# Kernel tuning notes

Hardware: AMD Instinct MI355X
Metric: run time of the kernel (lower is better)

The kernel has to match this reference:

```python
import jax, jax.numpy as jnp
import numpy as np
import math

D_MODEL = 1024
HEADS = 16
D_K = D_MODEL // HEADS
B, S = 4, 2048


def setup_inputs() -> dict:
    key = jax.random.key(0)
    ks = jax.random.split(key, 7)
    scale = 1.0 / math.sqrt(D_MODEL)
    inp = {
        "q": jax.random.normal(ks[0], (B, S, D_MODEL), dtype=jnp.float32),
        "k": jax.random.normal(ks[1], (B, S, D_MODEL), dtype=jnp.float32),
        "v": jax.random.normal(ks[2], (B, S, D_MODEL), dtype=jnp.float32),
        # Linear(d_model, d_model, bias=False) weights, stored [out, in] torch-style
        "W_q": jax.random.normal(ks[3], (D_MODEL, D_MODEL), dtype=jnp.float32) * scale,
        "W_k": jax.random.normal(ks[4], (D_MODEL, D_MODEL), dtype=jnp.float32) * scale,
        "W_v": jax.random.normal(ks[5], (D_MODEL, D_MODEL), dtype=jnp.float32) * scale,
        "W_o": jax.random.normal(ks[6], (D_MODEL, D_MODEL), dtype=jnp.float32) * scale,
    }
    return inp


def reference(q, k, v, W_q, W_k, W_v, W_o):
    # projections (torch Linear: x @ W.T)
    query = jnp.einsum("bsd,ed->bse", q, W_q)
    key_ = jnp.einsum("bsd,ed->bse", k, W_k)
    value = jnp.einsum("bsd,ed->bse", v, W_v)
    # split heads -> [B, H, S, d_k]
    def split(x):
        return x.reshape(B, S, HEADS, D_K).transpose(0, 2, 1, 3)
    Q, K, V = split(query), split(key_), split(value)
    # scaled dot-product attention, full [B,H,S,S] scores (naive, faithful)
    scores = jnp.einsum("bhqd,bhkd->bhqk", Q, K) / math.sqrt(D_K)
    attn = jax.nn.softmax(scores, axis=-1)
    x = jnp.einsum("bhqk,bhkd->bhqd", attn, V)
    x = x.transpose(0, 2, 1, 3).reshape(B, S, D_MODEL)
    return jnp.einsum("bsd,ed->bse", x, W_o)
```

## Files before the change

kernel.cpp:

```cpp
#include <hip/hip_runtime.h>
#include <stdint.h>

#define NHEAD 16
#define DKH 64
#define BBATCH 4
#define SEQ 2048
#define MROWS (BBATCH*SEQ)
#define DMODEL 1024

typedef __attribute__((ext_vector_type(8))) __bf16 bf16x8;
typedef __attribute__((ext_vector_type(4))) float f32x4;

__device__ __forceinline__ unsigned short f2bf(float x) {
  unsigned int u = __float_as_uint(x);
  u += 0x7FFFu + ((u >> 16) & 1u);
  return (unsigned short)(u >> 16);
}
__device__ __forceinline__ unsigned int pkbf(float a, float b) {
  return __builtin_amdgcn_perm(__float_as_uint(b) + 0x8000u,
                               __float_as_uint(a) + 0x8000u, 0x07060302u);
}
__device__ __forceinline__ unsigned int pkbf_t(float a, float b) {
  return __builtin_amdgcn_perm(__float_as_uint(b), __float_as_uint(a), 0x07060302u);
}
__device__ __forceinline__ void gl_lds16(const void* g, void* l) {
  __builtin_amdgcn_global_load_lds(
      (const __attribute__((address_space(1))) unsigned int*)g,
      (__attribute__((address_space(3))) unsigned int*)l, 16, 0, 0);
}
__device__ __forceinline__ f32x4 mfma16(bf16x8 a, bf16x8 b, f32x4 c) {
  return __builtin_amdgcn_mfma_f32_16x16x32_bf16(a, b, c, 0, 0, 0);
}

__global__ __launch_bounds__(256) void cvt_all(
    const float* __restrict__ s0, const float* __restrict__ s1,
    const float* __restrict__ s2, const float* __restrict__ s3,
    const float* __restrict__ s4, const float* __restrict__ s5,
    const float* __restrict__ s6,
    unsigned short* __restrict__ d0, unsigned short* __restrict__ d1,
    unsigned short* __restrict__ d2, unsigned short* __restrict__ d3,
    unsigned short* __restrict__ d4, unsigned short* __restrict__ d5,
    unsigned short* __restrict__ d6) {
  const int NB = 2097152;
  const int NW = 262144;
  int i = blockIdx.x * 256 + threadIdx.x;
  const float* src; unsigned short* dst; int off;
  if      (i < NB)          { src = s0; dst = d0; off = i; }
  else if (i < 2*NB)        { src = s1; dst = d1; off = i - NB; }
  else if (i < 3*NB)        { src = s2; dst = d2; off = i - 2*NB; }
  else if (i < 3*NB + NW)   { src = s3; dst = d3; off = i - 3*NB; }
  else if (i < 3*NB + 2*NW) { src = s4; dst = d4; off = i - 3*NB - NW; }
  else if (i < 3*NB + 3*NW) { src = s5; dst = d5; off = i - 3*NB - 2*NW; }
  else                      { src = s6; dst = d6; off = i - 3*NB - 3*NW; }
  float4 x = ((const float4*)src)[off];
  uint2 o; o.x = pkbf(x.x, x.y); o.y = pkbf(x.z, x.w);
  ((uint2*)dst)[off] = o;
}

__global__ __launch_bounds__(256, 2) void proj_gemm(
    const unsigned short* __restrict__ A0, const unsigned short* __restrict__ A1,
    const unsigned short* __restrict__ A2,
    const unsigned short* __restrict__ B0, const unsigned short* __restrict__ B1,
    const unsigned short* __restrict__ B2,
    unsigned short* __restrict__ O0, unsigned short* __restrict__ O1,
    unsigned short* __restrict__ O2) {
  __shared__ __align__(16) unsigned short smem[2][16384];
  const int z = blockIdx.z;
  const unsigned short* Ah = (z == 0) ? A0 : ((z == 1) ? A1 : A2);
  const unsigned short* Bh = (z == 0) ? B0 : ((z == 1) ? B1 : B2);
  unsigned short* outp = (z == 0) ? O0 : ((z == 1) ? O1 : O2);
  const int t = threadIdx.x;
  const int bm = blockIdx.x, bn = blockIdx.y;
  const int lane = t & 63, lm = lane & 15, quad = lane >> 4;
  const int w = t >> 6, wr = w >> 1, wc = w & 1;

  f32x4 acc[4][4];
#pragma unroll
  for (int i = 0; i < 4; ++i)
#pragma unroll
    for (int j = 0; j < 4; ++j) acc[i][j] = (f32x4){0.f, 0.f, 0.f, 0.f};

  auto stage = [&](int kk, int b) {
#pragma unroll
    for (int jj = 0; jj < 4; ++jj) {
      int cid = jj * 256 + t;
      int r = cid >> 3, c = cid & 7;
      int gcol = kk * 64 + ((c ^ (r & 7)) * 8);
      gl_lds16(Ah + (bm * 128 + r) * 1024 + gcol, &smem[b][cid * 8]);
      gl_lds16(Bh + (bn * 128 + r) * 1024 + gcol, &smem[b][8192 + cid * 8]);
    }
  };

  stage(0, 0);
  __syncthreads();

  for (int kk = 0; kk < 16; ++kk) {
    const int cur = kk & 1;
    if (kk < 15) stage(kk + 1, cur ^ 1);
    const unsigned short* sA = &smem[cur][0];
    const unsigned short* sB = &smem[cur][8192];
#pragma unroll
    for (int kc = 0; kc < 2; ++kc) {
      bf16x8 af[4], bf[4];
#pragma unroll
      for (int i = 0; i < 4; ++i) {
        int m = wr * 64 + i * 16 + lm;
        int nn = wc * 64 + i * 16 + lm;
        int slot = ((kc * 4 + quad) ^ (lm & 7)) * 8;
        af[i] = *(const bf16x8*)(sA + m * 64 + slot);
        bf[i] = *(const bf16x8*)(sB + nn * 64 + slot);
      }
#pragma unroll
      for (int i = 0; i < 4; ++i)
#pragma unroll
        for (int j = 0; j < 4; ++j) acc[i][j] = mfma16(af[i], bf[j], acc[i][j]);
    }
    __syncthreads();
  }

  if (z < 2) {
    float scale = (z == 0) ? 0.125f * 1.44269504f : 1.0f;
#pragma unroll
    for (int i = 0; i < 4; ++i)
#pragma unroll
      for (int j = 0; j < 4; ++j)
#pragma unroll
        for (int r = 0; r < 4; ++r) {
          int m = bm * 128 + wr * 64 + i * 16 + quad * 4 + r;
          int nn = bn * 128 + wc * 64 + j * 16 + lm;
          int b = m >> 11, s = m & 2047, h = nn >> 6, d = nn & 63;
          outp[((b * 16 + h) * 2048 + s) * 64 + d] = f2bf(acc[i][j][r] * scale);
        }
  } else {
    unsigned short* scr = &smem[0][0];
#pragma unroll
    for (int i = 0; i < 4; ++i)
#pragma unroll
      for (int j = 0; j < 4; ++j)
#pragma unroll
        for (int r = 0; r < 4; ++r) {
          int ml = wr * 64 + i * 16 + quad * 4 + r;
          int nl = wc * 64 + j * 16 + lm;
          scr[nl * 128 + (((ml >> 3) ^ (nl & 15)) << 3) + (ml & 7)] =
              f2bf(acc[i][j][r]);
        }
    __syncthreads();
    int nl = t >> 1, half = t & 1;
    int e = bn * 128 + nl, h = e >> 6, d = e & 63;
    int mg = bm * 128;
    int b = mg >> 11, s0 = mg & 2047;
    uint4* dstp = (uint4*)(outp + ((b * 16 + h) * 64 + d) * 2048 + s0);
#pragma unroll
    for (int u = 0; u < 8; ++u) {
      int c = half * 8 + u;
      int slot = c ^ (nl & 15);
      dstp[c] = *(const uint4*)(scr + nl * 128 + slot * 8);
    }
  }
}

__global__ __launch_bounds__(256, 4) void flash_attn(
    const unsigned short* __restrict__ Qw, const unsigned short* __restrict__ Kw,
    const unsigned short* __restrict__ Vt, unsigned short* __restrict__ Xw) {
  __shared__ __align__(16) unsigned short sK[2][64 * 64];
  __shared__ __align__(16) unsigned short sV[2][64 * 64];
  const int t = threadIdx.x;
  const int bh = (blockIdx.x << 3) | blockIdx.z;
  const int qt = blockIdx.y;
  const int lane = t & 63, lm = lane & 15, quad = lane >> 4;
  const int w = t >> 6;

  const unsigned short* gq = Qw + (long)bh * SEQ * 64 + (long)qt * 128 * 64;
  const unsigned short* gk = Kw + (long)bh * SEQ * 64;
  const unsigned short* gv = Vt + (long)bh * 64 * SEQ;

  bf16x8 qf[2][2];
#pragma unroll
  for (int i = 0; i < 2; ++i)
#pragma unroll
    for (int kc = 0; kc < 2; ++kc)
      qf[i][kc] = *(const bf16x8*)(gq + (w * 32 + i * 16 + lm) * 64 + kc * 32 + quad * 8);

  f32x4 o[2][4];
  f32x4 lacc[2];
#pragma unroll
  for (int i = 0; i < 2; ++i) {
    lacc[i] = (f32x4){0.f, 0.f, 0.f, 0.f};
#pragma unroll
    for (int nv = 0; nv < 4; ++nv) o[i][nv] = (f32x4){0.f, 0.f, 0.f, 0.f};
  }

  auto stage = [&](int kt, int b) {
#pragma unroll
    for (int is = 0; is < 2; ++is) {
      int cid = is * 256 + t;
      int rk = cid >> 3, ck = cid & 7;
      int srk = (rk & 3) | ((rk & 8) >> 1);
      gl_lds16(gk + kt * 64 * 64 + rk * 64 + ((ck ^ srk) * 8), &sK[b][cid * 8]);
      int rv = cid >> 3, cv = cid & 7;
      gl_lds16(gv + kt * 64 + rv * SEQ + ((cv ^ (rv & 7)) * 8), &sV[b][cid * 8]);
    }
  };

  uint4 ou; ou.x = ou.y = ou.z = ou.w = 0x3F803F80u;
  const bf16x8 ones = __builtin_bit_cast(bf16x8, ou);

  stage(0, 0);
  __syncthreads();

  for (int kt = 0; kt < 32; ++kt) {
    const int cur = kt & 1;
    if (kt < 31) stage(kt + 1, cur ^ 1);
    const unsigned short* sk = &sK[cur][0];
    const unsigned short* sv = &sV[cur][0];
#pragma unroll
    for (int p = 0; p < 2; ++p) {
      bf16x8 kf[2][2];
#pragma unroll
      for (int tt = 0; tt < 2; ++tt) {
        int g = p * 32 + 8 * (lm >> 2) + (lm & 3) + 4 * tt;
        int sg = (g & 3) | ((g & 8) >> 1);
        kf[tt][0] = *(const bf16x8*)(sk + g * 64 + ((quad ^ sg) * 8));
        kf[tt][1] = *(const bf16x8*)(sk + g * 64 + (((4 + quad) ^ sg) * 8));
      }
      bf16x8 pfrag[2];
#pragma unroll
      for (int i = 0; i < 2; ++i) {
        f32x4 s0 = (f32x4){0.f, 0.f, 0.f, 0.f};
        f32x4 s1 = (f32x4){0.f, 0.f, 0.f, 0.f};
        __builtin_amdgcn_s_setprio(1);
        s0 = mfma16(kf[0][0], qf[i][0], s0);
        s0 = mfma16(kf[0][1], qf[i][1], s0);
        s1 = mfma16(kf[1][0], qf[i][0], s1);
        s1 = mfma16(kf[1][1], qf[i][1], s1);
        __builtin_amdgcn_s_setprio(0);
        float p0[4], p1[4];
#pragma unroll
        for (int r = 0; r < 4; ++r) {
          p0[r] = __builtin_amdgcn_exp2f(s0[r]);
          p1[r] = __builtin_amdgcn_exp2f(s1[r]);
        }
        uint4 pw;
        pw.x = pkbf_t(p0[0], p0[1]); pw.y = pkbf_t(p0[2], p0[3]);
        pw.z = pkbf_t(p1[0], p1[1]); pw.w = pkbf_t(p1[2], p1[3]);
        pfrag[i] = __builtin_bit_cast(bf16x8, pw);
      }
      __builtin_amdgcn_s_setprio(1);
#pragma unroll
      for (int i = 0; i < 2; ++i) lacc[i] = mfma16(pfrag[i], ones, lacc[i]);
#pragma unroll
      for (int nv = 0; nv < 4; ++nv) {
        bf16x8 vb = *(const bf16x8*)(sv + (nv * 16 + lm) * 64 + (((p * 4 + quad) ^ (lm & 7)) * 8));
#pragma unroll
        for (int i = 0; i < 2; ++i) o[i][nv] = mfma16(pfrag[i], vb, o[i][nv]);
      }
      __builtin_amdgcn_s_setprio(0);
    }
    __syncthreads();
  }

  int b = bh >> 4, h = bh & 15;
#pragma unroll
  for (int i = 0; i < 2; ++i) {
    float inv[4];
#pragma unroll
    for (int r = 0; r < 4; ++r) inv[r] = __builtin_amdgcn_rcpf(lacc[i][r]);
#pragma unroll
    for (int nv = 0; nv < 4; ++nv)
#pragma unroll
      for (int r = 0; r < 4; ++r) {
        int q = qt * 128 + w * 32 + i * 16 + quad * 4 + r;
        int d = nv * 16 + lm;
        Xw[((long)(b * 2048 + q) * 16 + h) * 64 + d] = f2bf(o[i][nv][r] * inv[r]);
      }
  }
}

__global__ __launch_bounds__(256, 2) void out_gemm(
    const unsigned short* __restrict__ A, const unsigned short* __restrict__ Bw,
    float* __restrict__ C) {
  __shared__ __align__(16) unsigned short smem[2][16384];
  const int t = threadIdx.x;
  const int bm = blockIdx.x, bn = blockIdx.y;
  const int lane = t & 63, lm = lane & 15, quad = lane >> 4;
  const int w = t >> 6, wr = w >> 1, wc = w & 1;

  f32x4 acc[4][4];
#pragma unroll
  for (int i = 0; i < 4; ++i)
#pragma unroll
    for (int j = 0; j < 4; ++j) acc[i][j] = (f32x4){0.f, 0.f, 0.f, 0.f};

  auto stage = [&](int kk, int b) {
#pragma unroll
    for (int jj = 0; jj < 4; ++jj) {
      int cid = jj * 256 + t;
      int r = cid >> 3, c = cid & 7;
      int gcol = kk * 64 + ((c ^ (r & 7)) * 8);
      gl_lds16(A + (bm * 128 + r) * 1024 + gcol, &smem[b][cid * 8]);
      gl_lds16(Bw + (bn * 128 + r) * 1024 + gcol, &smem[b][8192 + cid * 8]);
    }
  };

  stage(0, 0);
  __syncthreads();

  for (int kk = 0; kk < 16; ++kk) {
    const int cur = kk & 1;
    if (kk < 15) stage(kk + 1, cur ^ 1);
    const unsigned short* sA = &smem[cur][0];
    const unsigned short* sB = &smem[cur][8192];
#pragma unroll
    for (int kc = 0; kc < 2; ++kc) {
      bf16x8 af[4], bf[4];
#pragma unroll
      for (int i = 0; i < 4; ++i) {
        int m = wr * 64 + i * 16 + lm;
        int nn = wc * 64 + i * 16 + lm;
        int slot = ((kc * 4 + quad) ^ (lm & 7)) * 8;
        af[i] = *(const bf16x8*)(sA + m * 64 + slot);
        bf[i] = *(const bf16x8*)(sB + nn * 64 + slot);
      }
#pragma unroll
      for (int i = 0; i < 4; ++i)
#pragma unroll
        for (int j = 0; j < 4; ++j) acc[i][j] = mfma16(af[i], bf[j], acc[i][j]);
    }
    __syncthreads();
  }
#pragma unroll
  for (int i = 0; i < 4; ++i)
#pragma unroll
    for (int j = 0; j < 4; ++j)
#pragma unroll
      for (int r = 0; r < 4; ++r) {
        int m = bm * 128 + wr * 64 + i * 16 + quad * 4 + r;
        int nn = bn * 128 + wc * 64 + j * 16 + lm;
        C[m * 1024 + nn] = acc[i][j][r];
      }
}

extern "C" void kernel_launch(void* const* d_in, const int* in_sizes, int n_in,
                              void* d_out, int out_size, void* d_ws, size_t ws_size,
                              hipStream_t stream) {
  const float* q  = (const float*)d_in[0];
  const float* k  = (const float*)d_in[1];
  const float* v  = (const float*)d_in[2];
  const float* Wq = (const float*)d_in[3];
  const float* Wk = (const float*)d_in[4];
  const float* Wv = (const float*)d_in[5];
  const float* Wo = (const float*)d_in[6];

  char* ws = (char*)d_ws;
  const size_t MK = (size_t)MROWS * DMODEL;
  const size_t KK = (size_t)DMODEL * DMODEL;
  size_t off = 0;
  auto nxt = [&](size_t elems) { unsigned short* p = (unsigned short*)(ws + off); off += elems * 2; return p; };
  unsigned short* q_b  = nxt(MK);
  unsigned short* k_b  = nxt(MK);
  unsigned short* v_b  = nxt(MK);
  unsigned short* Wq_b = nxt(KK);
  unsigned short* Wk_b = nxt(KK);
  unsigned short* Wv_b = nxt(KK);
  unsigned short* Wo_b = nxt(KK);
  unsigned short* Qw = nxt(MK);
  unsigned short* Kw = nxt(MK);
  unsigned short* Vt = nxt(MK);
  unsigned short* Xw = nxt(MK);
  (void)ws_size; (void)in_sizes; (void)n_in; (void)out_size;

  cvt_all<<<28672, 256, 0, stream>>>(q, k, v, Wq, Wk, Wv, Wo,
                                     q_b, k_b, v_b, Wq_b, Wk_b, Wv_b, Wo_b);
  proj_gemm<<<dim3(64, 8, 3), 256, 0, stream>>>(q_b, k_b, v_b,
                                                Wq_b, Wk_b, Wv_b,
                                                Qw, Kw, Vt);
  flash_attn<<<dim3(8, 16, 8), 256, 0, stream>>>(Qw, Kw, Vt, Xw);
  out_gemm<<<dim3(64, 8), 256, 0, stream>>>(Xw, Wo_b, (float*)d_out);
}
```

Baseline: 303.0 us.

## Fuse fp32-to-bf16 activation conversion into projection GEMM A-tile staging

```diff
diff --git a/kernel.cpp b/kernel.cpp
--- a/kernel.cpp
+++ b/kernel.cpp
@@ -32,41 +32,33 @@
   return __builtin_amdgcn_mfma_f32_16x16x32_bf16(a, b, c, 0, 0, 0);
 }
 
-__global__ __launch_bounds__(256) void cvt_all(
-    const float* __restrict__ s0, const float* __restrict__ s1,
-    const float* __restrict__ s2, const float* __restrict__ s3,
-    const float* __restrict__ s4, const float* __restrict__ s5,
-    const float* __restrict__ s6,
-    unsigned short* __restrict__ d0, unsigned short* __restrict__ d1,
-    unsigned short* __restrict__ d2, unsigned short* __restrict__ d3,
-    unsigned short* __restrict__ d4, unsigned short* __restrict__ d5,
-    unsigned short* __restrict__ d6) {
-  const int NB = 2097152;
+__global__ __launch_bounds__(256) void cvt_w(
+    const float* __restrict__ s3, const float* __restrict__ s4,
+    const float* __restrict__ s5, const float* __restrict__ s6,
+    unsigned short* __restrict__ d3, unsigned short* __restrict__ d4,
+    unsigned short* __restrict__ d5, unsigned short* __restrict__ d6) {
   const int NW = 262144;
   int i = blockIdx.x * 256 + threadIdx.x;
   const float* src; unsigned short* dst; int off;
-  if      (i < NB)          { src = s0; dst = d0; off = i; }
-  else if (i < 2*NB)        { src = s1; dst = d1; off = i - NB; }
-  else if (i < 3*NB)        { src = s2; dst = d2; off = i - 2*NB; }
-  else if (i < 3*NB + NW)   { src = s3; dst = d3; off = i - 3*NB; }
-  else if (i < 3*NB + 2*NW) { src = s4; dst = d4; off = i - 3*NB - NW; }
-  else if (i < 3*NB + 3*NW) { src = s5; dst = d5; off = i - 3*NB - 2*NW; }
-  else                      { src = s6; dst = d6; off = i - 3*NB - 3*NW; }
+  if      (i < NW)     { src = s3; dst = d3; off = i; }
+  else if (i < 2*NW)   { src = s4; dst = d4; off = i - NW; }
+  else if (i < 3*NW)   { src = s5; dst = d5; off = i - 2*NW; }
+  else                 { src = s6; dst = d6; off = i - 3*NW; }
   float4 x = ((const float4*)src)[off];
   uint2 o; o.x = pkbf(x.x, x.y); o.y = pkbf(x.z, x.w);
   ((uint2*)dst)[off] = o;
 }
 
 __global__ __launch_bounds__(256, 2) void proj_gemm(
-    const unsigned short* __restrict__ A0, const unsigned short* __restrict__ A1,
-    const unsigned short* __restrict__ A2,
+    const float* __restrict__ A0, const float* __restrict__ A1,
+    const float* __restrict__ A2,
     const unsigned short* __restrict__ B0, const unsigned short* __restrict__ B1,
     const unsigned short* __restrict__ B2,
     unsigned short* __restrict__ O0, unsigned short* __restrict__ O1,
     unsigned short* __restrict__ O2) {
   __shared__ __align__(16) unsigned short smem[2][16384];
   const int z = blockIdx.z;
-  const unsigned short* Ah = (z == 0) ? A0 : ((z == 1) ? A1 : A2);
+  const float* Ah = (z == 0) ? A0 : ((z == 1) ? A1 : A2);
   const unsigned short* Bh = (z == 0) ? B0 : ((z == 1) ? B1 : B2);
   unsigned short* outp = (z == 0) ? O0 : ((z == 1) ? O1 : O2);
   const int t = threadIdx.x;
@@ -80,23 +72,51 @@
 #pragma unroll
     for (int j = 0; j < 4; ++j) acc[i][j] = (f32x4){0.f, 0.f, 0.f, 0.f};
 
-  auto stage = [&](int kk, int b) {
+  float4 ar[8];
+  auto loadA = [&](int kk) {
 #pragma unroll
     for (int jj = 0; jj < 4; ++jj) {
       int cid = jj * 256 + t;
       int r = cid >> 3, c = cid & 7;
       int gcol = kk * 64 + ((c ^ (r & 7)) * 8);
-      gl_lds16(Ah + (bm * 128 + r) * 1024 + gcol, &smem[b][cid * 8]);
+      const float4* src = (const float4*)(Ah + (bm * 128 + r) * 1024 + gcol);
+      ar[2 * jj]     = src[0];
+      ar[2 * jj + 1] = src[1];
+    }
+  };
+  auto writeA = [&](int b) {
+#pragma unroll
+    for (int jj = 0; jj < 4; ++jj) {
+      int cid = jj * 256 + t;
+      uint4 wv;
+      wv.x = pkbf(ar[2 * jj].x,     ar[2 * jj].y);
+      wv.y = pkbf(ar[2 * jj].z,     ar[2 * jj].w);
+      wv.z = pkbf(ar[2 * jj + 1].x, ar[2 * jj + 1].y);
+      wv.w = pkbf(ar[2 * jj + 1].z, ar[2 * jj + 1].w);
+      *(uint4*)(&smem[b][cid * 8]) = wv;
+    }
+  };
+  auto stageB = [&](int kk, int b) {
+#pragma unroll
+    for (int jj = 0; jj < 4; ++jj) {
+      int cid = jj * 256 + t;
+      int r = cid >> 3, c = cid & 7;
+      int gcol = kk * 64 + ((c ^ (r & 7)) * 8);
       gl_lds16(Bh + (bn * 128 + r) * 1024 + gcol, &smem[b][8192 + cid * 8]);
     }
   };
 
-  stage(0, 0);
+  loadA(0);
+  stageB(0, 0);
+  writeA(0);
   __syncthreads();
 
   for (int kk = 0; kk < 16; ++kk) {
     const int cur = kk & 1;
-    if (kk < 15) stage(kk + 1, cur ^ 1);
+    if (kk < 15) {
+      loadA(kk + 1);
+      stageB(kk + 1, cur ^ 1);
+    }
     const unsigned short* sA = &smem[cur][0];
     const unsigned short* sB = &smem[cur][8192];
 #pragma unroll
@@ -115,6 +135,7 @@
 #pragma unroll
         for (int j = 0; j < 4; ++j) acc[i][j] = mfma16(af[i], bf[j], acc[i][j]);
     }
+    if (kk < 15) writeA(cur ^ 1);
     __syncthreads();
   }
 
@@ -190,16 +211,19 @@
     for (int nv = 0; nv < 4; ++nv) o[i][nv] = (f32x4){0.f, 0.f, 0.f, 0.f};
   }
 
+  const int cid0 = t, cid1 = 256 + t;
+  const int rk0 = cid0 >> 3, ck0 = cid0 & 7;
+  const int rk1 = cid1 >> 3, ck1 = cid1 & 7;
+  const int kof0 = rk0 * 64 + (((ck0 ^ ((rk0 & 3) | ((rk0 & 8) >> 1)))) * 8);
+  const int kof1 = rk1 * 64 + (((ck1 ^ ((rk1 & 3) | ((rk1 & 8) >> 1)))) * 8);
+  const int vof0 = rk0 * SEQ + ((ck0 ^ (rk0 & 7)) * 8);
+  const int vof1 = rk1 * SEQ + ((ck1 ^ (rk1 & 7)) * 8);
+
   auto stage = [&](int kt, int b) {
-#pragma unroll
-    for (int is = 0; is < 2; ++is) {
-      int cid = is * 256 + t;
-      int rk = cid >> 3, ck = cid & 7;
-      int srk = (rk & 3) | ((rk & 8) >> 1);
-      gl_lds16(gk + kt * 64 * 64 + rk * 64 + ((ck ^ srk) * 8), &sK[b][cid * 8]);
-      int rv = cid >> 3, cv = cid & 7;
-      gl_lds16(gv + kt * 64 + rv * SEQ + ((cv ^ (rv & 7)) * 8), &sV[b][cid * 8]);
-    }
+    gl_lds16(gk + kt * 64 * 64 + kof0, &sK[b][cid0 * 8]);
+    gl_lds16(gk + kt * 64 * 64 + kof1, &sK[b][cid1 * 8]);
+    gl_lds16(gv + kt * 64 + vof0, &sV[b][cid0 * 8]);
+    gl_lds16(gv + kt * 64 + vof1, &sV[b][cid1 * 8]);
   };
 
   uint4 ou; ou.x = ou.y = ou.z = ou.w = 0x3F803F80u;
@@ -208,6 +232,7 @@
   stage(0, 0);
   __syncthreads();
 
+#pragma unroll 2
   for (int kt = 0; kt < 32; ++kt) {
     const int cur = kt & 1;
     if (kt < 31) stage(kt + 1, cur ^ 1);
@@ -356,9 +381,6 @@
   const size_t KK = (size_t)DMODEL * DMODEL;
   size_t off = 0;
   auto nxt = [&](size_t elems) { unsigned short* p = (unsigned short*)(ws + off); off += elems * 2; return p; };
-  unsigned short* q_b  = nxt(MK);
-  unsigned short* k_b  = nxt(MK);
-  unsigned short* v_b  = nxt(MK);
   unsigned short* Wq_b = nxt(KK);
   unsigned short* Wk_b = nxt(KK);
   unsigned short* Wv_b = nxt(KK);
@@ -369,9 +391,8 @@
   unsigned short* Xw = nxt(MK);
   (void)ws_size; (void)in_sizes; (void)n_in; (void)out_size;
 
-  cvt_all<<<28672, 256, 0, stream>>>(q, k, v, Wq, Wk, Wv, Wo,
-                                     q_b, k_b, v_b, Wq_b, Wk_b, Wv_b, Wo_b);
-  proj_gemm<<<dim3(64, 8, 3), 256, 0, stream>>>(q_b, k_b, v_b,
+  cvt_w<<<4096, 256, 0, stream>>>(Wq, Wk, Wv, Wo, Wq_b, Wk_b, Wv_b, Wo_b);
+  proj_gemm<<<dim3(64, 8, 3), 256, 0, stream>>>(q, k, v,
                                                 Wq_b, Wk_b, Wv_b,
                                                 Qw, Kw, Vt);
   flash_attn<<<dim3(8, 16, 8), 256, 0, stream>>>(Qw, Kw, Vt, Xw);
```

Measured after the change: 350.0 us. 1.15x slower.

## Give each wave private K/V staging buffers to drop block-wide barriers in attention

Applied to the files above, without the earlier changes.

```diff
diff --git a/kernel.cpp b/kernel.cpp
--- a/kernel.cpp
+++ b/kernel.cpp
@@ -159,11 +159,11 @@
   }
 }
 
-__global__ __launch_bounds__(256, 4) void flash_attn(
+__global__ __launch_bounds__(256, 2) void flash_attn(
     const unsigned short* __restrict__ Qw, const unsigned short* __restrict__ Kw,
     const unsigned short* __restrict__ Vt, unsigned short* __restrict__ Xw) {
-  __shared__ __align__(16) unsigned short sK[2][64 * 64];
-  __shared__ __align__(16) unsigned short sV[2][64 * 64];
+  __shared__ __align__(16) unsigned short sK[4][2][32 * 64];
+  __shared__ __align__(16) unsigned short sV[4][2][64 * 32];
   const int t = threadIdx.x;
   const int bh = (blockIdx.x << 3) | blockIdx.z;
   const int qt = blockIdx.y;
@@ -190,73 +190,85 @@
     for (int nv = 0; nv < 4; ++nv) o[i][nv] = (f32x4){0.f, 0.f, 0.f, 0.f};
   }
 
-  auto stage = [&](int kt, int b) {
-#pragma unroll
-    for (int is = 0; is < 2; ++is) {
-      int cid = is * 256 + t;
+  unsigned short* k0 = &sK[w][0][0];
+  unsigned short* k1 = &sK[w][1][0];
+  unsigned short* v0 = &sV[w][0][0];
+  unsigned short* v1 = &sV[w][1][0];
+
+  auto stage = [&](int kt, unsigned short* dK, unsigned short* dV) {
+#pragma unroll
+    for (int is = 0; is < 4; ++is) {
+      int cid = is * 64 + lane;
       int rk = cid >> 3, ck = cid & 7;
       int srk = (rk & 3) | ((rk & 8) >> 1);
-      gl_lds16(gk + kt * 64 * 64 + rk * 64 + ((ck ^ srk) * 8), &sK[b][cid * 8]);
-      int rv = cid >> 3, cv = cid & 7;
-      gl_lds16(gv + kt * 64 + rv * SEQ + ((cv ^ (rv & 7)) * 8), &sV[b][cid * 8]);
+      gl_lds16(gk + kt * 32 * 64 + rk * 64 + ((ck ^ srk) * 8), dK + cid * 8);
+    }
+#pragma unroll
+    for (int is = 0; is < 4; ++is) {
+      int cid = is * 64 + lane;
+      int rv = cid >> 2, cv = cid & 3;
+      gl_lds16(gv + kt * 32 + rv * SEQ + ((cv ^ (rv & 3)) * 8), dV + cid * 8);
     }
   };
 
   uint4 ou; ou.x = ou.y = ou.z = ou.w = 0x3F803F80u;
   const bf16x8 ones = __builtin_bit_cast(bf16x8, ou);
 
-  stage(0, 0);
-  __syncthreads();
-
-  for (int kt = 0; kt < 32; ++kt) {
+  stage(0, k0, v0);
+  stage(1, k1, v1);
+  asm volatile("s_waitcnt vmcnt(8)" ::: "memory");
+
+#pragma unroll 2
+  for (int kt = 0; kt < 64; ++kt) {
     const int cur = kt & 1;
-    if (kt < 31) stage(kt + 1, cur ^ 1);
-    const unsigned short* sk = &sK[cur][0];
-    const unsigned short* sv = &sV[cur][0];
-#pragma unroll
-    for (int p = 0; p < 2; ++p) {
-      bf16x8 kf[2][2];
-#pragma unroll
-      for (int tt = 0; tt < 2; ++tt) {
-        int g = p * 32 + 8 * (lm >> 2) + (lm & 3) + 4 * tt;
-        int sg = (g & 3) | ((g & 8) >> 1);
-        kf[tt][0] = *(const bf16x8*)(sk + g * 64 + ((quad ^ sg) * 8));
-        kf[tt][1] = *(const bf16x8*)(sk + g * 64 + (((4 + quad) ^ sg) * 8));
-      }
-      bf16x8 pfrag[2];
-#pragma unroll
-      for (int i = 0; i < 2; ++i) {
-        f32x4 s0 = (f32x4){0.f, 0.f, 0.f, 0.f};
-        f32x4 s1 = (f32x4){0.f, 0.f, 0.f, 0.f};
-        __builtin_amdgcn_s_setprio(1);
-        s0 = mfma16(kf[0][0], qf[i][0], s0);
-        s0 = mfma16(kf[0][1], qf[i][1], s0);
-        s1 = mfma16(kf[1][0], qf[i][0], s1);
-        s1 = mfma16(kf[1][1], qf[i][1], s1);
-        __builtin_amdgcn_s_setprio(0);
-        float p0[4], p1[4];
-#pragma unroll
-        for (int r = 0; r < 4; ++r) {
-          p0[r] = __builtin_amdgcn_exp2f(s0[r]);
-          p1[r] = __builtin_amdgcn_exp2f(s1[r]);
-        }
-        uint4 pw;
-        pw.x = pkbf_t(p0[0], p0[1]); pw.y = pkbf_t(p0[2], p0[3]);
-        pw.z = pkbf_t(p1[0], p1[1]); pw.w = pkbf_t(p1[2], p1[3]);
-        pfrag[i] = __builtin_bit_cast(bf16x8, pw);
-      }
-      __builtin_amdgcn_s_setprio(1);
-#pragma unroll
-      for (int i = 0; i < 2; ++i) lacc[i] = mfma16(pfrag[i], ones, lacc[i]);
-#pragma unroll
-      for (int nv = 0; nv < 4; ++nv) {
-        bf16x8 vb = *(const bf16x8*)(sv + (nv * 16 + lm) * 64 + (((p * 4 + quad) ^ (lm & 7)) * 8));
-#pragma unroll
-        for (int i = 0; i < 2; ++i) o[i][nv] = mfma16(pfrag[i], vb, o[i][nv]);
-      }
-      __builtin_amdgcn_s_setprio(0);
-    }
-    __syncthreads();
+    const unsigned short* sk = cur ? k1 : k0;
+    const unsigned short* sv = cur ? v1 : v0;
+
+    bf16x8 kf[2][2];
+#pragma unroll
+    for (int tt = 0; tt < 2; ++tt) {
+      int g = 8 * (lm >> 2) + (lm & 3) + 4 * tt;
+      int sg = (g & 3) | ((g & 8) >> 1);
+      kf[tt][0] = *(const bf16x8*)(sk + g * 64 + ((quad ^ sg) * 8));
+      kf[tt][1] = *(const bf16x8*)(sk + g * 64 + (((4 + quad) ^ sg) * 8));
+    }
+    bf16x8 pfrag[2];
+#pragma unroll
+    for (int i = 0; i < 2; ++i) {
+      f32x4 s0 = (f32x4){0.f, 0.f, 0.f, 0.f};
+      f32x4 s1 = (f32x4){0.f, 0.f, 0.f, 0.f};
+      s0 = mfma16(kf[0][0], qf[i][0], s0);
+      s0 = mfma16(kf[0][1], qf[i][1], s0);
+      s1 = mfma16(kf[1][0], qf[i][0], s1);
+      s1 = mfma16(kf[1][1], qf[i][1], s1);
+      float p0[4], p1[4];
+#pragma unroll
+      for (int r = 0; r < 4; ++r) {
+        p0[r] = __builtin_amdgcn_exp2f(s0[r]);
+        p1[r] = __builtin_amdgcn_exp2f(s1[r]);
+      }
+      uint4 pw;
+      pw.x = pkbf_t(p0[0], p0[1]); pw.y = pkbf_t(p0[2], p0[3]);
+      pw.z = pkbf_t(p1[0], p1[1]); pw.w = pkbf_t(p1[2], p1[3]);
+      pfrag[i] = __builtin_bit_cast(bf16x8, pw);
+    }
+#pragma unroll
+    for (int i = 0; i < 2; ++i) lacc[i] = mfma16(pfrag[i], ones, lacc[i]);
+#pragma unroll
+    for (int nv = 0; nv < 4; ++nv) {
+      int d = nv * 16 + lm;
+      bf16x8 vb = *(const bf16x8*)(sv + d * 32 + ((quad ^ (d & 3)) * 8));
+      o[0][nv] = mfma16(pfrag[0], vb, o[0][nv]);
+      o[1][nv] = mfma16(pfrag[1], vb, o[1][nv]);
+    }
+
+    if (kt < 62) {
+      asm volatile("s_waitcnt lgkmcnt(0)" ::: "memory");
+      stage(kt + 2, cur ? k1 : k0, cur ? v1 : v0);
+      asm volatile("s_waitcnt vmcnt(8)" ::: "memory");
+    } else {
+      asm volatile("s_waitcnt vmcnt(0)" ::: "memory");
+    }
   }
 
   int b = bh >> 4, h = bh & 15;
@@ -366,7 +378,7 @@
   unsigned short* Qw = nxt(MK);
   unsigned short* Kw = nxt(MK);
   unsigned short* Vt = nxt(MK);
-  unsigned short* Xw = nxt(MK);
+  unsigned short* Xw = q_b;
   (void)ws_size; (void)in_sizes; (void)n_in; (void)out_size;
 
   cvt_all<<<28672, 256, 0, stream>>>(q, k, v, Wq, Wk, Wv, Wo,
```

After: 327.7 us. +8.1%, slower.
